# Kernel optimization log

Hardware: AMD Instinct MI355X
Metric: run time of the kernel (lower is better)

Reference implementation:

```python
import jax, jax.numpy as jnp
import numpy as np

NEG_MASK = -999.0  # matches masked_fill_(-999) in the torch source

def setup_inputs() -> dict:
    key = jax.random.key(0)
    ks = jax.random.split(key, 8)
    B, N, D = 4, 2048, 768      # batch, nodes, in_dim
    H, Do = 6, 128              # att_head, out_dim (D == H*Do)
    feat_in = jax.random.normal(ks[0], (B, N, D), dtype=jnp.float32)
    adj = jax.random.randint(ks[1], (B, N, N), 0, 2).astype(jnp.int32)
    W = jax.random.normal(ks[2], (H, D, Do), dtype=jnp.float32) * (1.0 / np.sqrt(D))
    b = jnp.zeros((Do,), dtype=jnp.float32)
    w_src = jax.random.normal(ks[3], (H, Do, 1), dtype=jnp.float32) * (1.0 / np.sqrt(Do))
    w_dst = jax.random.normal(ks[4], (H, Do, 1), dtype=jnp.float32) * (1.0 / np.sqrt(Do))
    H_w = jax.random.normal(ks[5], (D, D), dtype=jnp.float32) * (1.0 / np.sqrt(D))
    H_b = jnp.zeros((D,), dtype=jnp.float32)
    return {"feat_in": feat_in, "adj": adj, "W": W, "b": b,
            "w_src": w_src, "w_dst": w_dst, "H_w": H_w, "H_b": H_b}

def reference(feat_in, adj, W, b, w_src, w_dst, H_w, H_b):
    leaky_alpha = 0.2
    B, N, D = feat_in.shape
    Hh = W.shape[0]
    # per-head projection: [B, H, N, Do]
    h = jnp.einsum('bni,hio->bhno', feat_in, W)
    th = jnp.tanh(h)
    attn_src = jnp.einsum('bhno,hoz->bhnz', th, w_src)  # [B,H,N,1]
    attn_dst = jnp.einsum('bhno,hoz->bhnz', th, w_dst)  # [B,H,N,1]
    # additive scores: src_i + dst_j -> [B,H,N,N]
    attn = attn_src + jnp.swapaxes(attn_dst, -1, -2)
    attn = jnp.where(attn >= 0, attn, leaky_alpha * attn)
    mask = (adj == 0)[:, None, :, :]  # [B,1,N,N]
    attn = jnp.where(mask, NEG_MASK, attn)
    attn = jax.nn.softmax(attn, axis=-1)
    feat_out = jnp.einsum('bhnm,bhmo->bhno', attn, h) + b  # [B,H,N,Do]
    feat_out = jnp.swapaxes(feat_out, 1, 2).reshape(B, N, -1)  # [B,N,H*Do]
    feat_out = jax.nn.elu(feat_out)
    gate = jax.nn.sigmoid(feat_in @ H_w.T + H_b)
    out = gate * feat_out + (1.0 - gate) * feat_in
    return out
```

## Files before the change

### kernel.cpp

```cpp
#include <hip/hip_runtime.h>
#include <hip/hip_bf16.h>

#define B_ 4
#define N_ 2048
#define D_ 768
#define H_ 6
#define Do_ 128
#define M_ (B_*N_)
#define C2_ (2*D_)
#define SROW 49152

typedef __attribute__((ext_vector_type(8))) short bf16x8;
typedef __attribute__((ext_vector_type(4))) float f32x4;
typedef __attribute__((ext_vector_type(4))) int int4v;
typedef __attribute__((ext_vector_type(2))) int int2v;
typedef __attribute__((ext_vector_type(4))) float float4v;
typedef __attribute__((ext_vector_type(4))) unsigned short ushort4v;

__device__ __forceinline__ float b2f(short s){
    unsigned u = ((unsigned)(unsigned short)s) << 16;
    return __builtin_bit_cast(float, u);
}
__device__ __forceinline__ short f2b(float f){
    unsigned u = __builtin_bit_cast(unsigned, f);
    unsigned r = (u + 0x7fffu + ((u >> 16) & 1u)) >> 16;
    return (short)r;
}
__device__ __forceinline__ int pk2(float a, float b){
    unsigned ua = __builtin_bit_cast(unsigned, a) + 0x8000u;
    unsigned ub = __builtin_bit_cast(unsigned, b) + 0x8000u;
    return (int)__builtin_amdgcn_perm(ub, ua, 0x07060302u);
}
__device__ __forceinline__ float fast_tanh(float x){
    float a = fabsf(x);
    float e = __expf(-2.0f * a);
    float t = (1.0f - e) / (1.0f + e);
    return copysignf(t, x);
}

__global__ __launch_bounds__(256) void k_prep_pack(const float* __restrict__ W,
                                                   const float* __restrict__ Hw,
                                                   const int* __restrict__ adj,
                                                   short* __restrict__ bmat,
                                                   unsigned char* __restrict__ pk){
    int bid = blockIdx.x, t = threadIdx.x;
    if (bid < C2_){
        int c = bid;
        if (c < D_){
            int hd = c >> 7, o = c & 127;
            const float* wp = W + hd*D_*Do_ + o;
            for (int k = t; k < D_; k += 256) bmat[c*D_ + k] = f2b(wp[k*Do_]);
        } else {
            int d = c - D_;
            const float* hp = Hw + d*D_;
            for (int k = t; k < D_; k += 256) bmat[c*D_ + k] = f2b(hp[k]);
        }
    } else {
        int g = (bid - C2_)*256 + t;
        const int* ap = adj + (size_t)g*8;
        int4v a0 = *(const int4v*)ap;
        int4v a1 = *(const int4v*)(ap + 4);
        unsigned by = 0;
        #pragma unroll
        for (int i = 0; i < 4; i++){
            by |= (a0[i] ? 1u : 0u) << i;
            by |= (a1[i] ? 1u : 0u) << (i + 4);
        }
        pk[g] = (unsigned char)by;
    }
}

__global__ __launch_bounds__(256) void k_gemm(const float* __restrict__ A,
                                              const short* __restrict__ Bm,
                                              short* __restrict__ ht,
                                              float* outg){
    __shared__ short As[128][72];
    __shared__ short Bs[128][72];
    int tid = threadIdx.x;
    int mBase = blockIdx.y * 128, cBase = blockIdx.x * 128;
    int wave = tid >> 6, lane = tid & 63, q = lane >> 4, nL = lane & 15;
    int wr = (wave >> 1) * 64, wc = (wave & 1) * 64;
    f32x4 acc[4][4] = {};
    for (int kk = 0; kk < D_; kk += 64){
        __syncthreads();
        #pragma unroll
        for (int i = 0; i < 8; i++){
            int idx = tid + i*256;
            int row = idx >> 4, c4 = (idx & 15) * 4;
            float4v av = *(const float4v*)&A[(mBase+row)*D_ + kk + c4];
            int2v w; w[0] = pk2(av[0], av[1]); w[1] = pk2(av[2], av[3]);
            *(int2v*)&As[row][c4] = w;
        }
        #pragma unroll
        for (int i = 0; i < 4; i++){
            int idx = tid + i*256;
            int row = idx >> 3, cs = (idx & 7) * 8;
            *(int4v*)&Bs[row][cs] = *(const int4v*)&Bm[(cBase+row)*D_ + kk + cs];
        }
        __syncthreads();
        #pragma unroll
        for (int k2 = 0; k2 < 64; k2 += 32){
            bf16x8 aF[4], bF[4];
            #pragma unroll
            for (int rt = 0; rt < 4; rt++) aF[rt] = *(const bf16x8*)&As[wr + rt*16 + nL][k2 + q*8];
            #pragma unroll
            for (int ct = 0; ct < 4; ct++) bF[ct] = *(const bf16x8*)&Bs[wc + ct*16 + nL][k2 + q*8];
            #pragma unroll
            for (int rt = 0; rt < 4; rt++)
                #pragma unroll
                for (int ct = 0; ct < 4; ct++)
                    acc[rt][ct] = __builtin_amdgcn_mfma_f32_16x16x32_bf16(aF[rt], bF[ct], acc[rt][ct], 0, 0, 0);
        }
    }
    if (cBase < D_){
        int hd = cBase >> 7;
        #pragma unroll
        for (int rt = 0; rt < 4; rt++){
            #pragma unroll
            for (int ct = 0; ct < 4; ct++){
                int o  = (wc + ct*16 + nL) & 127;
                int m0 = mBase + wr + rt*16 + q*4;
                int b = m0 >> 11, n0 = m0 & 2047;
                ushort4v v;
                #pragma unroll
                for (int r = 0; r < 4; r++) v[r] = (unsigned short)f2b(acc[rt][ct][r]);
                *(ushort4v*)&ht[((b*H_ + hd)*Do_ + o)*N_ + n0] = v;
            }
        }
    } else {
        #pragma unroll
        for (int rt = 0; rt < 4; rt++){
            #pragma unroll
            for (int ct = 0; ct < 4; ct++){
                int d  = cBase - D_ + wc + ct*16 + nL;
                int m0 = mBase + wr + rt*16 + q*4;
                #pragma unroll
                for (int r = 0; r < 4; r++) outg[(size_t)(m0 + r)*D_ + d] = acc[rt][ct][r];
            }
        }
    }
}

__global__ __launch_bounds__(256) void k_stats(const short* __restrict__ ht,
                                               const float* __restrict__ wsrc,
                                               const float* __restrict__ wdst,
                                               float* __restrict__ srcP,
                                               float* __restrict__ dstP){
    int g = blockIdx.x * 256 + threadIdx.x;
    int y = blockIdx.y, o0 = y * 32;
    int bh = g >> 11, n = g & 2047;
    int hd = bh % H_;
    const short* hp = ht + bh*Do_*N_ + n + o0*N_;
    const float* ws = wsrc + hd*Do_ + o0;
    const float* wd = wdst + hd*Do_ + o0;
    float as = 0.f, ad = 0.f;
    for (int o = 0; o < 32; o++){
        float t = fast_tanh(b2f(hp[o*N_]));
        as += t * ws[o];
        ad += t * wd[o];
    }
    srcP[y*SROW + g] = as; dstP[y*SROW + g] = ad;
}

struct StageS {
    float E1[2048];
    float E2[2048];
    unsigned pkw[64*65];
};
struct RedS { float red[2][64][37]; };
union LdsU { StageS s; RedS r; };
__global__ __launch_bounds__(256) void k_pv(const unsigned char* __restrict__ pkG,
                                            const float* __restrict__ srcP,
                                            const float* __restrict__ dstP,
                                            const short* __restrict__ ht,
                                            const float* __restrict__ feat_in,
                                            const float* __restrict__ bias,
                                            const float* __restrict__ Hb,
                                            float* outg){
    __shared__ LdsU U;
    int itile = blockIdx.x, hd = blockIdx.y, b = blockIdx.z;
    int tid = threadIdx.x, wave = tid >> 6, lane = tid & 63, q = lane >> 4, nL = lane & 15;
    int rh = wave >> 1, kh = wave & 1;
    int r0 = itile * 64;
    int bh = b*H_ + hd;
    {
        const float4v* g0 = (const float4v*)(dstP + bh*N_);
        const float4v* g1 = (const float4v*)(dstP + SROW + bh*N_);
        const float4v* g2 = (const float4v*)(dstP + 2*SROW + bh*N_);
        const float4v* g3 = (const float4v*)(dstP + 3*SROW + bh*N_);
        #pragma unroll
        for (int h = 0; h < 2; h++){
            int c4 = tid*2 + h;
            float4v d = g0[c4] + g1[c4] + g2[c4] + g3[c4];
            #pragma unroll
            for (int t = 0; t < 4; t++){
                U.s.E1[c4*4 + t] = __expf(d[t]);
                U.s.E2[c4*4 + t] = __expf(0.2f * d[t]);
            }
        }
        const unsigned* pg = (const unsigned*)(pkG + (size_t)(b*N_ + r0) * (N_/8));
        #pragma unroll
        for (int k = 0; k < 16; k++){
            int idx = tid + k*256;
            U.s.pkw[(idx >> 6)*65 + (idx & 63)] = pg[idx];
        }
    }
    __syncthreads();
    int rowL0 = rh*32 + nL, rowL1 = rowL0 + 16;
    int gi0 = bh*N_ + r0 + rowL0, gi1 = bh*N_ + r0 + rowL1;
    float s0 = srcP[gi0] + srcP[SROW+gi0] + srcP[2*SROW+gi0] + srcP[3*SROW+gi0];
    float s1 = srcP[gi1] + srcP[SROW+gi1] + srcP[2*SROW+gi1] + srcP[3*SROW+gi1];
    float e1r0 = __expf(s0), e2r0 = __expf(0.2f*s0);
    float e1r1 = __expf(s1), e2r1 = __expf(0.2f*s1);
    bf16x8 vone;
    #pragma unroll
    for (int t = 0; t < 8; t++) vone[t] = (short)0x3F80;
    const short* hp = ht + bh*Do_*N_;
    f32x4 acc[2][8] = {};
    f32x4 accl0 = {}, accl1 = {};
    int base0 = rowL0*65, base1 = rowL1*65;
    int jEnd = kh*1024 + 1024;
    for (int j0 = kh*1024; j0 < jEnd; j0 += 32){
        unsigned by0 = (U.s.pkw[base0 + (j0 >> 5)] >> (q*8)) & 0xFF;
        unsigned by1 = (U.s.pkw[base1 + (j0 >> 5)] >> (q*8)) & 0xFF;
        int kb = j0 + q*8;
        float4v E1a = *(const float4v*)&U.s.E1[kb];
        float4v E1b = *(const float4v*)&U.s.E1[kb + 4];
        float4v E2a = *(const float4v*)&U.s.E2[kb];
        float4v E2b = *(const float4v*)&U.s.E2[kb + 4];
        float p0[8], p1[8];
        #pragma unroll
        for (int t = 0; t < 8; t++){
            float E1t = t < 4 ? E1a[t] : E1b[t-4];
            float E2t = t < 4 ? E2a[t] : E2b[t-4];
            float a0 = fmaxf(e1r0*E1t, e2r0*E2t);
            float a1 = fmaxf(e1r1*E1t, e2r1*E2t);
            p0[t] = ((by0 >> t) & 1u) ? a0 : 0.0f;
            p1[t] = ((by1 >> t) & 1u) ? a1 : 0.0f;
        }
        int4v pi0, pi1;
        #pragma unroll
        for (int tp = 0; tp < 4; tp++){
            pi0[tp] = pk2(p0[2*tp], p0[2*tp+1]);
            pi1[tp] = pk2(p1[2*tp], p1[2*tp+1]);
        }
        bf16x8 pf0 = __builtin_bit_cast(bf16x8, pi0);
        bf16x8 pf1 = __builtin_bit_cast(bf16x8, pi1);
        #pragma unroll
        for (int ct = 0; ct < 8; ct++){
            bf16x8 bF = *(const bf16x8*)&hp[(ct*16 + nL)*N_ + kb];
            acc[0][ct] = __builtin_amdgcn_mfma_f32_16x16x32_bf16(pf0, bF, acc[0][ct], 0, 0, 0);
            acc[1][ct] = __builtin_amdgcn_mfma_f32_16x16x32_bf16(pf1, bF, acc[1][ct], 0, 0, 0);
        }
        accl0 = __builtin_amdgcn_mfma_f32_16x16x32_bf16(pf0, vone, accl0, 0, 0, 0);
        accl1 = __builtin_amdgcn_mfma_f32_16x16x32_bf16(pf1, vone, accl1, 0, 0, 0);
    }
    __syncthreads();
    if (kh == 1){
        #pragma unroll
        for (int ct = 0; ct < 8; ct++)
            #pragma unroll
            for (int r = 0; r < 4; r++) U.r.red[rh][lane][ct*4 + r] = acc[0][ct][r];
        #pragma unroll
        for (int r = 0; r < 4; r++) U.r.red[rh][lane][32 + r] = accl0[r];
    }
    __syncthreads();
    if (kh == 0){
        #pragma unroll
        for (int ct = 0; ct < 8; ct++)
            #pragma unroll
            for (int r = 0; r < 4; r++) acc[0][ct][r] += U.r.red[rh][lane][ct*4 + r];
        #pragma unroll
        for (int r = 0; r < 4; r++) accl0[r] += U.r.red[rh][lane][32 + r];
    }
    __syncthreads();
    if (kh == 0){
        #pragma unroll
        for (int ct = 0; ct < 8; ct++)
            #pragma unroll
            for (int r = 0; r < 4; r++) U.r.red[rh][lane][ct*4 + r] = acc[1][ct][r];
        #pragma unroll
        for (int r = 0; r < 4; r++) U.r.red[rh][lane][32 + r] = accl1[r];
    }
    __syncthreads();
    if (kh == 1){
        #pragma unroll
        for (int ct = 0; ct < 8; ct++)
            #pragma unroll
            for (int r = 0; r < 4; r++) acc[1][ct][r] += U.r.red[rh][lane][ct*4 + r];
        #pragma unroll
        for (int r = 0; r < 4; r++) accl1[r] += U.r.red[rh][lane][32 + r];
    }
    {
        int f = kh;
        f32x4 accl = f ? accl1 : accl0;
        #pragma unroll
        for (int r = 0; r < 4; r++){
            int i = r0 + rh*32 + f*16 + q*4 + r;
            float invl = 1.0f / accl[r];
            size_t base = (size_t)(b*N_ + i)*D_ + hd*Do_;
            #pragma unroll
            for (int ct = 0; ct < 8; ct++){
                int o = ct*16 + nL;
                float v = acc[f][ct][r]*invl + bias[o];
                float e = v > 0.f ? v : __expf(v) - 1.0f;
                float gl = outg[base + o] + Hb[hd*Do_ + o];
                float g = 1.0f / (1.0f + __expf(-gl));
                float fi = feat_in[base + o];
                outg[base + o] = g*e + (1.0f - g)*fi;
            }
        }
    }
}

extern "C" void kernel_launch(void* const* d_in, const int* in_sizes, int n_in,
                              void* d_out, int out_size, void* d_ws, size_t ws_size,
                              hipStream_t stream){
    const float* feat = (const float*)d_in[0];
    const int*   adj  = (const int*)  d_in[1];
    const float* W    = (const float*)d_in[2];
    const float* bias = (const float*)d_in[3];
    const float* wsrc = (const float*)d_in[4];
    const float* wdst = (const float*)d_in[5];
    const float* Hw   = (const float*)d_in[6];
    const float* Hb   = (const float*)d_in[7];
    float* out = (float*)d_out;
    char* ws = (char*)d_ws;
    short* bmat = (short*)(ws);
    short* ht   = (short*)(ws + 2359296);
    float* srcP = (float*)(ws + 14942208);
    float* dstP = (float*)(ws + 15728640);
    unsigned char* pk = (unsigned char*)(ws + 16515072);

    hipLaunchKernelGGL(k_prep_pack, dim3(C2_ + 8192), dim3(256), 0, stream, W, Hw, adj, bmat, pk);
    hipLaunchKernelGGL(k_gemm,      dim3(12, 64),     dim3(256), 0, stream, feat, bmat, ht, out);
    hipLaunchKernelGGL(k_stats,     dim3(192, 4),     dim3(256), 0, stream, ht, wsrc, wdst, srcP, dstP);
    hipLaunchKernelGGL(k_pv,        dim3(32, 6, 4),   dim3(256), 0, stream, pk, srcP, dstP,
                       ht, feat, bias, Hb, out);
}
```

Before: 317.6 us.

## Pre-convert feat to bf16 and use direct global-to-LDS loads in GEMM

The prep kernel now also converts feat_in to bf16 in workspace. When the workspace is large enough, a new GEMM kernel loads bf16 tiles straight into LDS with global_load_lds and an XOR-swizzled layout, which removes the per-iteration fp32-to-bf16 conversion and register staging. Both the GEMM and PV kernels remap block IDs so that blocks scheduled together map to neighbouring tiles (likely an XCD-aware swizzle), to improve cache locality. The cost is an extra pass over feat and an extra workspace buffer, and the old path is kept as a fallback for small workspaces.

```diff
diff --git a/kernel.cpp b/kernel.cpp
--- a/kernel.cpp
+++ b/kernel.cpp
@@ -37,11 +37,18 @@
     float t = (1.0f - e) / (1.0f + e);
     return copysignf(t, x);
 }
+__device__ __forceinline__ void gload_lds16(const void* g, void* l){
+    __builtin_amdgcn_global_load_lds((const __attribute__((address_space(1))) unsigned int*)g,
+                                     (__attribute__((address_space(3))) unsigned int*)l,
+                                     16, 0, 0);
+}
 
 __global__ __launch_bounds__(256) void k_prep_pack(const float* __restrict__ W,
                                                    const float* __restrict__ Hw,
+                                                   const float* __restrict__ feat,
                                                    const int* __restrict__ adj,
                                                    short* __restrict__ bmat,
+                                                   short* __restrict__ featbf,
                                                    unsigned char* __restrict__ pk){
     int bid = blockIdx.x, t = threadIdx.x;
     if (bid < C2_){
@@ -55,7 +62,7 @@
             const float* hp = Hw + d*D_;
             for (int k = t; k < D_; k += 256) bmat[c*D_ + k] = f2b(hp[k]);
         }
-    } else {
+    } else if (bid < C2_ + 8192){
         int g = (bid - C2_)*256 + t;
         const int* ap = adj + (size_t)g*8;
         int4v a0 = *(const int4v*)ap;
@@ -67,13 +74,99 @@
             by |= (a1[i] ? 1u : 0u) << (i + 4);
         }
         pk[g] = (unsigned char)by;
-    }
-}
-
-__global__ __launch_bounds__(256) void k_gemm(const float* __restrict__ A,
-                                              const short* __restrict__ Bm,
-                                              short* __restrict__ ht,
-                                              float* outg){
+    } else {
+        int g = (bid - C2_ - 8192)*2048 + t*8;
+        float4v a0 = *(const float4v*)&feat[g];
+        float4v a1 = *(const float4v*)&feat[g + 4];
+        int4v w;
+        w[0] = pk2(a0[0], a0[1]); w[1] = pk2(a0[2], a0[3]);
+        w[2] = pk2(a1[0], a1[1]); w[3] = pk2(a1[2], a1[3]);
+        *(int4v*)&featbf[g] = w;
+    }
+}
+
+__global__ __launch_bounds__(256) void k_gemm_bf(const short* __restrict__ Abf,
+                                                 const short* __restrict__ Bm,
+                                                 short* __restrict__ ht,
+                                                 float* outg){
+    __shared__ short As[128*64];
+    __shared__ short Bs[128*64];
+    int lid = blockIdx.x;
+    int nid = (lid & 7)*96 + (lid >> 3);
+    int bx = nid % 12, by = nid / 12;
+    int mBase = by * 128, cBase = bx * 128;
+    int tid = threadIdx.x, wave = tid >> 6, lane = tid & 63, q = lane >> 4, nL = lane & 15;
+    int wr = (wave >> 1) * 64, wc = (wave & 1) * 64;
+    int srow = tid >> 3;
+    int sc16 = (tid & 7) ^ (srow & 7);
+    const short* aSrc = Abf + (size_t)(mBase + srow)*D_ + sc16*8;
+    const short* bSrc = Bm  + (size_t)(cBase + srow)*D_ + sc16*8;
+    short* aDst = &As[wave*512];
+    short* bDst = &Bs[wave*512];
+    f32x4 acc[4][4] = {};
+    for (int kk = 0; kk < D_; kk += 64){
+        __syncthreads();
+        #pragma unroll
+        for (int i = 0; i < 4; i++)
+            gload_lds16(aSrc + (size_t)i*32*D_ + kk, aDst + i*2048);
+        #pragma unroll
+        for (int i = 0; i < 4; i++)
+            gload_lds16(bSrc + (size_t)i*32*D_ + kk, bDst + i*2048);
+        __syncthreads();
+        #pragma unroll
+        for (int k2 = 0; k2 < 64; k2 += 32){
+            bf16x8 aF[4], bF[4];
+            int cb = (k2 >> 3) + q;
+            #pragma unroll
+            for (int rt = 0; rt < 4; rt++){
+                int r = wr + rt*16 + nL;
+                aF[rt] = *(const bf16x8*)&As[r*64 + ((cb ^ (r & 7)) * 8)];
+            }
+            #pragma unroll
+            for (int ct = 0; ct < 4; ct++){
+                int r = wc + ct*16 + nL;
+                bF[ct] = *(const bf16x8*)&Bs[r*64 + ((cb ^ (r & 7)) * 8)];
+            }
+            #pragma unroll
+            for (int rt = 0; rt < 4; rt++)
+                #pragma unroll
+                for (int ct = 0; ct < 4; ct++)
+                    acc[rt][ct] = __builtin_amdgcn_mfma_f32_16x16x32_bf16(aF[rt], bF[ct], acc[rt][ct], 0, 0, 0);
+        }
+    }
+    if (cBase < D_){
+        int hd = cBase >> 7;
+        #pragma unroll
+        for (int rt = 0; rt < 4; rt++){
+            #pragma unroll
+            for (int ct = 0; ct < 4; ct++){
+                int o  = (wc + ct*16 + nL) & 127;
+                int m0 = mBase + wr + rt*16 + q*4;
+                int b = m0 >> 11, n0 = m0 & 2047;
+                ushort4v v;
+                #pragma unroll
+                for (int r = 0; r < 4; r++) v[r] = (unsigned short)f2b(acc[rt][ct][r]);
+                *(ushort4v*)&ht[((b*H_ + hd)*Do_ + o)*N_ + n0] = v;
+            }
+        }
+    } else {
+        #pragma unroll
+        for (int rt = 0; rt < 4; rt++){
+            #pragma unroll
+            for (int ct = 0; ct < 4; ct++){
+                int d  = cBase - D_ + wc + ct*16 + nL;
+                int m0 = mBase + wr + rt*16 + q*4;
+                #pragma unroll
+                for (int r = 0; r < 4; r++) outg[(size_t)(m0 + r)*D_ + d] = acc[rt][ct][r];
+            }
+        }
+    }
+}
+
+__global__ __launch_bounds__(256) void k_gemm_f32(const float* __restrict__ A,
+                                                  const short* __restrict__ Bm,
+                                                  short* __restrict__ ht,
+                                                  float* outg){
     __shared__ short As[128][72];
     __shared__ short Bs[128][72];
     int tid = threadIdx.x;
@@ -178,7 +271,10 @@
                                             const float* __restrict__ Hb,
                                             float* outg){
     __shared__ LdsU U;
-    int itile = blockIdx.x, hd = blockIdx.y, b = blockIdx.z;
+    int lid = blockIdx.x;
+    int nid = (lid & 7)*96 + (lid >> 3);
+    int itile = nid & 31;
+    int hd = (nid >> 5) % 6, b = nid / 192;
     int tid = threadIdx.x, wave = tid >> 6, lane = tid & 63, q = lane >> 4, nL = lane & 15;
     int rh = wave >> 1, kh = wave & 1;
     int r0 = itile * 64;
@@ -331,10 +427,17 @@
     float* srcP = (float*)(ws + 14942208);
     float* dstP = (float*)(ws + 15728640);
     unsigned char* pk = (unsigned char*)(ws + 16515072);
-
-    hipLaunchKernelGGL(k_prep_pack, dim3(C2_ + 8192), dim3(256), 0, stream, W, Hw, adj, bmat, pk);
-    hipLaunchKernelGGL(k_gemm,      dim3(12, 64),     dim3(256), 0, stream, feat, bmat, ht, out);
-    hipLaunchKernelGGL(k_stats,     dim3(192, 4),     dim3(256), 0, stream, ht, wsrc, wdst, srcP, dstP);
-    hipLaunchKernelGGL(k_pv,        dim3(32, 6, 4),   dim3(256), 0, stream, pk, srcP, dstP,
+    short* featbf = (short*)(ws + 18612224);
+    bool big = ws_size >= (size_t)31195136;
+
+    int prepGrid = C2_ + 8192 + (big ? 3072 : 0);
+    hipLaunchKernelGGL(k_prep_pack, dim3(prepGrid), dim3(256), 0, stream,
+                       W, Hw, feat, adj, bmat, featbf, pk);
+    if (big)
+        hipLaunchKernelGGL(k_gemm_bf,  dim3(768),    dim3(256), 0, stream, featbf, bmat, ht, out);
+    else
+        hipLaunchKernelGGL(k_gemm_f32, dim3(12, 64), dim3(256), 0, stream, feat, bmat, ht, out);
+    hipLaunchKernelGGL(k_stats, dim3(192, 4), dim3(256), 0, stream, ht, wsrc, wdst, srcP, dstP);
+    hipLaunchKernelGGL(k_pv,    dim3(768),    dim3(256), 0, stream, pk, srcP, dstP,
                        ht, feat, bias, Hb, out);
 }
```

Result: faster. 303.2 us (-4.5%).

## Tile ht into 32-node blocks and remap k_pv blocks across XCDs

Applied to the files above, without the earlier changes.

Changes the bf16 transposed projection buffer from [bh][o][n] to a blocked [bh][n/32][o][32] layout, so each k_pv MFMA B-fragment load for a 32-column step reads a contiguous 8KB chunk rather than rows strided by N. The k_pv grid is flattened and remapped so that consecutive hardware block ids spread across the 8 XCDs, while blocks sharing a (b,head) are grouped on one XCD to improve L2 reuse of ht and masks. The epilogue is split into static branches so acc indexing stays compile-time, which avoids dynamic register indexing. The gemm and stats kernels are updated to write and read the new layout.

```diff
diff --git a/kernel.cpp b/kernel.cpp
--- a/kernel.cpp
+++ b/kernel.cpp
@@ -37,6 +37,8 @@
     float t = (1.0f - e) / (1.0f + e);
     return copysignf(t, x);
 }
+
+#define HT_IDX(bh, n, o) ((((size_t)((bh)*64 + ((n) >> 5))*128 + (o))*32) + ((n) & 31))
 
 __global__ __launch_bounds__(256) void k_prep_pack(const float* __restrict__ W,
                                                    const float* __restrict__ Hw,
@@ -121,10 +123,11 @@
                 int o  = (wc + ct*16 + nL) & 127;
                 int m0 = mBase + wr + rt*16 + q*4;
                 int b = m0 >> 11, n0 = m0 & 2047;
+                int bh = b*H_ + hd;
                 ushort4v v;
                 #pragma unroll
                 for (int r = 0; r < 4; r++) v[r] = (unsigned short)f2b(acc[rt][ct][r]);
-                *(ushort4v*)&ht[((b*H_ + hd)*Do_ + o)*N_ + n0] = v;
+                *(ushort4v*)&ht[HT_IDX(bh, n0, o)] = v;
             }
         }
     } else {
@@ -150,12 +153,12 @@
     int y = blockIdx.y, o0 = y * 32;
     int bh = g >> 11, n = g & 2047;
     int hd = bh % H_;
-    const short* hp = ht + bh*Do_*N_ + n + o0*N_;
+    const short* hp = ht + HT_IDX(bh, n, o0);
     const float* ws = wsrc + hd*Do_ + o0;
     const float* wd = wdst + hd*Do_ + o0;
     float as = 0.f, ad = 0.f;
     for (int o = 0; o < 32; o++){
-        float t = fast_tanh(b2f(hp[o*N_]));
+        float t = fast_tanh(b2f(hp[o*32]));
         as += t * ws[o];
         ad += t * wd[o];
     }
@@ -169,6 +172,27 @@
 };
 struct RedS { float red[2][64][37]; };
 union LdsU { StageS s; RedS r; };
+
+#define PV_EPILOGUE(ACC, ACCL, FOFF)                                          \
+    {                                                                         \
+        _Pragma("unroll")                                                     \
+        for (int r = 0; r < 4; r++){                                          \
+            int i = r0 + rh*32 + (FOFF) + q*4 + r;                            \
+            float invl = 1.0f / (ACCL)[r];                                    \
+            size_t baseO = (size_t)(b*N_ + i)*D_ + hd*Do_;                    \
+            _Pragma("unroll")                                                 \
+            for (int ct = 0; ct < 8; ct++){                                   \
+                int o = ct*16 + nL;                                           \
+                float v = (ACC)[ct][r]*invl + bias[o];                        \
+                float e = v > 0.f ? v : __expf(v) - 1.0f;                     \
+                float gl = outg[baseO + o] + Hb[hd*Do_ + o];                  \
+                float g = 1.0f / (1.0f + __expf(-gl));                        \
+                float fi = feat_in[baseO + o];                                \
+                outg[baseO + o] = g*e + (1.0f - g)*fi;                        \
+            }                                                                 \
+        }                                                                     \
+    }
+
 __global__ __launch_bounds__(256) void k_pv(const unsigned char* __restrict__ pkG,
                                             const float* __restrict__ srcP,
                                             const float* __restrict__ dstP,
@@ -178,7 +202,10 @@
                                             const float* __restrict__ Hb,
                                             float* outg){
     __shared__ LdsU U;
-    int itile = blockIdx.x, hd = blockIdx.y, b = blockIdx.z;
+    int lid = blockIdx.x;
+    int nid = (lid & 7)*96 + (lid >> 3);
+    int itile = nid & 31;
+    int hd = (nid >> 5) % 6, b = nid / 192;
     int tid = threadIdx.x, wave = tid >> 6, lane = tid & 63, q = lane >> 4, nL = lane & 15;
     int rh = wave >> 1, kh = wave & 1;
     int r0 = itile * 64;
@@ -215,7 +242,7 @@
     bf16x8 vone;
     #pragma unroll
     for (int t = 0; t < 8; t++) vone[t] = (short)0x3F80;
-    const short* hp = ht + bh*Do_*N_;
+    const short* hp = ht + (size_t)bh*262144;
     f32x4 acc[2][8] = {};
     f32x4 accl0 = {}, accl1 = {};
     int base0 = rowL0*65, base1 = rowL1*65;
@@ -224,6 +251,7 @@
         unsigned by0 = (U.s.pkw[base0 + (j0 >> 5)] >> (q*8)) & 0xFF;
         unsigned by1 = (U.s.pkw[base1 + (j0 >> 5)] >> (q*8)) & 0xFF;
         int kb = j0 + q*8;
+        const short* hj = hp + (size_t)(j0 >> 5)*4096 + q*8;
         float4v E1a = *(const float4v*)&U.s.E1[kb];
         float4v E1b = *(const float4v*)&U.s.E1[kb + 4];
         float4v E2a = *(const float4v*)&U.s.E2[kb];
@@ -248,7 +276,7 @@
         bf16x8 pf1 = __builtin_bit_cast(bf16x8, pi1);
         #pragma unroll
         for (int ct = 0; ct < 8; ct++){
-            bf16x8 bF = *(const bf16x8*)&hp[(ct*16 + nL)*N_ + kb];
+            bf16x8 bF = *(const bf16x8*)&hj[(ct*16 + nL)*32];
             acc[0][ct] = __builtin_amdgcn_mfma_f32_16x16x32_bf16(pf0, bF, acc[0][ct], 0, 0, 0);
             acc[1][ct] = __builtin_amdgcn_mfma_f32_16x16x32_bf16(pf1, bF, acc[1][ct], 0, 0, 0);
         }
@@ -291,25 +319,10 @@
         #pragma unroll
         for (int r = 0; r < 4; r++) accl1[r] += U.r.red[rh][lane][32 + r];
     }
-    {
-        int f = kh;
-        f32x4 accl = f ? accl1 : accl0;
-        #pragma unroll
-        for (int r = 0; r < 4; r++){
-            int i = r0 + rh*32 + f*16 + q*4 + r;
-            float invl = 1.0f / accl[r];
-            size_t base = (size_t)(b*N_ + i)*D_ + hd*Do_;
-            #pragma unroll
-            for (int ct = 0; ct < 8; ct++){
-                int o = ct*16 + nL;
-                float v = acc[f][ct][r]*invl + bias[o];
-                float e = v > 0.f ? v : __expf(v) - 1.0f;
-                float gl = outg[base + o] + Hb[hd*Do_ + o];
-                float g = 1.0f / (1.0f + __expf(-gl));
-                float fi = feat_in[base + o];
-                outg[base + o] = g*e + (1.0f - g)*fi;
-            }
-        }
+    if (kh == 0){
+        PV_EPILOGUE(acc[0], accl0, 0)
+    } else {
+        PV_EPILOGUE(acc[1], accl1, 16)
     }
 }
 
@@ -335,6 +348,6 @@
     hipLaunchKernelGGL(k_prep_pack, dim3(C2_ + 8192), dim3(256), 0, stream, W, Hw, adj, bmat, pk);
     hipLaunchKernelGGL(k_gemm,      dim3(12, 64),     dim3(256), 0, stream, feat, bmat, ht, out);
     hipLaunchKernelGGL(k_stats,     dim3(192, 4),     dim3(256), 0, stream, ht, wsrc, wdst, srcP, dstP);
-    hipLaunchKernelGGL(k_pv,        dim3(32, 6, 4),   dim3(256), 0, stream, pk, srcP, dstP,
+    hipLaunchKernelGGL(k_pv,        dim3(768),        dim3(256), 0, stream, pk, srcP, dstP,
                        ht, feat, bias, Hb, out);
 }
```

After: 269.7 us. -15.1%, faster.
